# Optimization experiments

Measured on AMD Instinct MI355X. Metric: run time of the kernel, lower is better.

Reference implementation:

```python
import jax, jax.numpy as jnp
import numpy as np

GATE_SLOPE = 10.0
ALPHA = 0.8


def setup_inputs() -> dict:
    key = jax.random.key(0)
    k0, k1, k2, k3, k4, k5 = jax.random.split(key, 6)
    B, I, O, NB = 512, 128, 64, 8
    x = jax.random.normal(k0, (B, I), dtype=jnp.float32)
    k = jax.random.uniform(k1, (I, O, NB), dtype=jnp.float32) * 2.0 + 0.5
    Ec = jax.random.uniform(k2, (I, O, NB), dtype=jnp.float32) * 2.0 + 0.5
    Ps = jax.random.uniform(k3, (I, O, NB), dtype=jnp.float32) * 1.5 + 0.5
    bias = jax.random.normal(k4, (I, O, NB), dtype=jnp.float32) * 0.1
    coef = jax.random.normal(k5, (I, O, NB), dtype=jnp.float32)
    return {"x": x, "k": k, "Ec": Ec, "Ps": Ps, "bias": bias, "coef": coef}


def reference(x, k, Ec, Ps, bias, coef):
    # x: [B, I]; params: [I, O, NB]
    xe = x[:, :, None, None]  # [B, I, 1, 1], broadcasts against [I, O, NB]
    # The torch loop writes prev_x = x_sample each iteration, so sample b sees
    # x[b-1] as prev (x[-1] = 0 from the initial buffer). branch_sign is never
    # written back, so branch_snap == 1 always. prev is detached in torch.
    prev = jnp.concatenate([jnp.zeros_like(xe[:1]), xe[:-1]], axis=0)
    prev = jax.lax.stop_gradient(prev)

    is_moving_up = jax.nn.sigmoid(GATE_SLOPE * (xe - prev))          # [B,I,1,1]
    crossed_pos = jax.nn.sigmoid(GATE_SLOPE * (xe - Ec))             # [B,I,O,NB]
    crossed_neg = jax.nn.sigmoid(GATE_SLOPE * (-xe - Ec))            # [B,I,O,NB]
    switch_up = is_moving_up * crossed_pos
    switch_lo = (1.0 - is_moving_up) * crossed_neg
    # target = su*1 + sl*(-1) + (1 - su - sl)*branch_snap, branch_snap = 1
    target = switch_up - switch_lo + (1.0 - switch_up - switch_lo)
    branch_momentum = ALPHA + (1.0 - ALPHA) * target                 # alpha*1 + (1-alpha)*target
    basis = Ps * jnp.tanh(k * (xe + Ec * branch_momentum)) + bias    # [B,I,O,NB]
    return jnp.einsum('bion,ion->bo', basis, coef)                   # sum over (I, NB)
```

## Files before the change

### kernel.cpp

```cpp
#include <hip/hip_runtime.h>


#define GATE_C 14.426950408889634f
#define TANH_C 2.8853900817779268f

typedef float f32x2 __attribute__((ext_vector_type(2)));
typedef float f32x4 __attribute__((ext_vector_type(4)));
typedef int   i32x2 __attribute__((ext_vector_type(2)));

constexpr int B = 512, I = 128, O = 64, NB = 8, BT = 32, TILES = 2;
constexpr int BP = BT / 2;

__device__ __forceinline__ f32x2 pk_rcp1(f32x2 d) {
  i32x2 yi = (i32x2)(0x7EF127EA) - __builtin_bit_cast(i32x2, d);
  f32x2 y = __builtin_bit_cast(f32x2, yi);
  return y * __builtin_elementwise_fma(-d, y, (f32x2)(2.f));
}
__device__ __forceinline__ f32x2 pk_rcp2(f32x2 d) {
  i32x2 yi = (i32x2)(0x7EF127EA) - __builtin_bit_cast(i32x2, d);
  f32x2 y = __builtin_bit_cast(f32x2, yi);
  y = y * __builtin_elementwise_fma(-d, y, (f32x2)(2.f));
  return y * __builtin_elementwise_fma(-d, y, (f32x2)(2.f));
}
__device__ __forceinline__ f32x2 pk_exp2s(f32x2 t) {
  f32x2 r;
  r.x = __int_as_float((int)fmaf(t.x, 8388608.f, 1064866805.f));
  r.y = __int_as_float((int)fmaf(t.y, 8388608.f, 1064866805.f));
  return r;
}

__global__ __launch_bounds__(1024, 4) void fe_main(
    const float* __restrict__ x, const float* __restrict__ k,
    const float* __restrict__ Ec, const float* __restrict__ Ps,
    const float* __restrict__ bias, const float* __restrict__ coef,
    float* __restrict__ out)
{
  __shared__ f32x4 pl[I][NB];
  __shared__ f32x4 xp[I][BP];
  __shared__ f32x4 racc[16][8];
  __shared__ float red[16];

  const int tid = threadIdx.x;
  const int o   = blockIdx.y;
  const int n   = tid & 7;
  const int bpl = (tid >> 3) & 7;
  const int w   = tid >> 6;

  {
    const int i = tid >> 3, nn = tid & 7;
    const int g = (i * O + o) * NB + nn;
    const float E = Ec[g], K = k[g], P = Ps[g], C = coef[g], Bs = bias[g];
    const float pc = P * C;
    pl[i][nn] = (f32x4){E, E * GATE_C, K * TANH_C, pc};
    float pbase = fmaf(Bs, C, pc);
    #pragma unroll
    for (int m = 1; m < 64; m <<= 1) pbase += __shfl_xor(pbase, m);
    if ((tid & 63) == 0) red[w] = pbase;
  }

  #define PAIR(ACC, Q) {                                                     \
    const f32x2 xx = Q.lo, cc = Q.hi;                                        \
    const f32x2 ta = __builtin_elementwise_fma(xx, (f32x2)(GATE_C),          \
                                               (f32x2)(p.y));                \
    const f32x2 d1 = pk_exp2s(ta) + (f32x2)(1.f);                            \
    const f32x2 sg = pk_rcp1(d1);                    \
    const f32x2 bm = __builtin_elementwise_fma(cc, sg, (f32x2)(1.f));        \
    const f32x2 inr = __builtin_elementwise_fma((f32x2)(p.x), bm, xx);       \
    const f32x2 tb = (f32x2)(p.z) * inr;                                     \
    const f32x2 d2 = pk_exp2s(tb) + (f32x2)(1.f);                            \
    const f32x2 r = pk_rcp2(d2);                                             \
    ACC = __builtin_elementwise_fma((f32x2)(p.w), r, ACC); }

  for (int t = 0; t < TILES; ++t) {
    const int b0 = blockIdx.x * (BT * TILES) + t * BT;
    __syncthreads();

    for (int e = tid; e < I * BP; e += 1024) {
      const int bq = e & 15, i = e >> 4;
      const int re = b0 + 2 * bq;
      const float xe = x[re * I + i];
      const float xo = x[(re + 1) * I + i];
      const float xm = (re == 0) ? 0.f : x[(re - 1) * I + i];
      const float ce = -0.4f * __builtin_amdgcn_rcpf(
          1.f + __builtin_amdgcn_exp2f(GATE_C * (xe - xm)));
      const float co = -0.4f * __builtin_amdgcn_rcpf(
          1.f + __builtin_amdgcn_exp2f(GATE_C * (xo - xe)));
      xp[i][bq] = (f32x4){xe, xo, ce, co};
    }
    __syncthreads();

    f32x2 accL = (f32x2)(0.f), accH = (f32x2)(0.f);
    #pragma unroll
    for (int it = 0; it < 8; ++it) {
      const int i = w * 8 + it;
      const f32x4 p  = pl[i][n];
      const f32x4 qL = xp[i][bpl];
      const f32x4 qH = xp[i][bpl + 8];
      PAIR(accL, qL)
      PAIR(accH, qH)
    }

    #pragma unroll
    for (int m = 1; m < 8; m <<= 1) {
      accL.x += __shfl_xor(accL.x, m); accL.y += __shfl_xor(accL.y, m);
      accH.x += __shfl_xor(accH.x, m); accH.y += __shfl_xor(accH.y, m);
    }
    if (n == 0) racc[w][bpl] = (f32x4){accL.x, accL.y, accH.x, accH.y};
    __syncthreads();

    if (tid < 32) {
      const int pr = tid >> 1, sel = tid & 1;
      const int bq = pr & 7, hi = (pr >> 3) * 2;
      float s = 0.f;
      #pragma unroll
      for (int ww = 0; ww < 16; ++ww)
        s += ((const float*)&racc[ww][bq])[hi + sel];
      float base = 0.f;
      #pragma unroll
      for (int q = 0; q < 16; ++q) base += red[q];
      out[(b0 + tid) * O + o] = fmaf(-2.f, s, base);
    }
  }
  #undef PAIR
}

extern "C" void kernel_launch(void* const* d_in, const int* in_sizes, int n_in,
                              void* d_out, int out_size, void* d_ws, size_t ws_size,
                              hipStream_t stream) {
  const float* x    = (const float*)d_in[0];
  const float* k    = (const float*)d_in[1];
  const float* Ec   = (const float*)d_in[2];
  const float* Ps   = (const float*)d_in[3];
  const float* bias = (const float*)d_in[4];
  const float* coef = (const float*)d_in[5];
  float* out = (float*)d_out;

  dim3 grid(B / (BT * TILES), O);
  fe_main<<<grid, 1024, 0, stream>>>(x, k, Ec, Ps, bias, coef, out);
}
```

Baseline: 26.00 us.

## Double-buffer x tiles with register prefetch and process four tiles per block

Each block now handles four batch tiles instead of two, so the per-block parameter staging and base reduction are spread over more work. The x tile and its gate terms go into a double-buffered shared array: loads for the next tile are issued into registers before the current compute, then written to the other buffer afterwards. This removes one barrier per tile and hides global-load latency behind compute. In exchange the grid is halved, which leaves fewer blocks per CU, and the kernel uses more shared memory and registers.

```diff
diff --git a/kernel.cpp b/kernel.cpp
--- a/kernel.cpp
+++ b/kernel.cpp
@@ -8,7 +8,7 @@
 typedef float f32x4 __attribute__((ext_vector_type(4)));
 typedef int   i32x2 __attribute__((ext_vector_type(2)));
 
-constexpr int B = 512, I = 128, O = 64, NB = 8, BT = 32, TILES = 2;
+constexpr int B = 512, I = 128, O = 64, NB = 8, BT = 32, TILES = 4;
 constexpr int BP = BT / 2;
 
 __device__ __forceinline__ f32x2 pk_rcp1(f32x2 d) {
@@ -36,12 +36,13 @@
     float* __restrict__ out)
 {
   __shared__ f32x4 pl[I][NB];
-  __shared__ f32x4 xp[I][BP];
-  __shared__ f32x4 racc[16][8];
+  __shared__ f32x4 xp[2][I][BP];
+  __shared__ f32x4 racc[2][16][8];
   __shared__ float red[16];
 
   const int tid = threadIdx.x;
   const int o   = blockIdx.y;
+  const int bbase = blockIdx.x * (BT * TILES);
   const int n   = tid & 7;
   const int bpl = (tid >> 3) & 7;
   const int w   = tid >> 6;
@@ -58,6 +59,27 @@
     if ((tid & 63) == 0) red[w] = pbase;
   }
 
+  const int sbq = tid & 15;
+  const int si0 = tid >> 4;
+  const int si1 = si0 + 64;
+
+  {
+    #pragma unroll
+    for (int h = 0; h < 2; ++h) {
+      const int i = h ? si1 : si0;
+      const int re = bbase + 2 * sbq;
+      const float xe = x[re * I + i];
+      const float xo = x[(re + 1) * I + i];
+      const float xm = (re == 0) ? 0.f : x[(re - 1) * I + i];
+      const float ce = -0.4f * __builtin_amdgcn_rcpf(
+          1.f + __builtin_amdgcn_exp2f(GATE_C * (xe - xm)));
+      const float co = -0.4f * __builtin_amdgcn_rcpf(
+          1.f + __builtin_amdgcn_exp2f(GATE_C * (xo - xe)));
+      xp[0][i][sbq] = (f32x4){xe, xo, ce, co};
+    }
+  }
+  __syncthreads();
+
   #define PAIR(ACC, Q) {                                                     \
     const f32x2 xx = Q.lo, cc = Q.hi;                                        \
     const f32x2 ta = __builtin_elementwise_fma(xx, (f32x2)(GATE_C),          \
@@ -72,30 +94,24 @@
     ACC = __builtin_elementwise_fma((f32x2)(p.w), r, ACC); }
 
   for (int t = 0; t < TILES; ++t) {
-    const int b0 = blockIdx.x * (BT * TILES) + t * BT;
-    __syncthreads();
+    const int cur = t & 1;
 
-    for (int e = tid; e < I * BP; e += 1024) {
-      const int bq = e & 15, i = e >> 4;
-      const int re = b0 + 2 * bq;
-      const float xe = x[re * I + i];
-      const float xo = x[(re + 1) * I + i];
-      const float xm = (re == 0) ? 0.f : x[(re - 1) * I + i];
-      const float ce = -0.4f * __builtin_amdgcn_rcpf(
-          1.f + __builtin_amdgcn_exp2f(GATE_C * (xe - xm)));
-      const float co = -0.4f * __builtin_amdgcn_rcpf(
-          1.f + __builtin_amdgcn_exp2f(GATE_C * (xo - xe)));
-      xp[i][bq] = (f32x4){xe, xo, ce, co};
+    float pxe0, pxo0, pxm0, pxe1, pxo1, pxm1;
+    if (t + 1 < TILES) {
+      const int re = bbase + (t + 1) * BT + 2 * sbq;
+      pxe0 = x[re * I + si0]; pxo0 = x[(re + 1) * I + si0];
+      pxm0 = x[(re - 1) * I + si0];
+      pxe1 = x[re * I + si1]; pxo1 = x[(re + 1) * I + si1];
+      pxm1 = x[(re - 1) * I + si1];
     }
-    __syncthreads();
 
     f32x2 accL = (f32x2)(0.f), accH = (f32x2)(0.f);
     #pragma unroll
     for (int it = 0; it < 8; ++it) {
       const int i = w * 8 + it;
       const f32x4 p  = pl[i][n];
-      const f32x4 qL = xp[i][bpl];
-      const f32x4 qH = xp[i][bpl + 8];
+      const f32x4 qL = xp[cur][i][bpl];
+      const f32x4 qH = xp[cur][i][bpl + 8];
       PAIR(accL, qL)
       PAIR(accH, qH)
     }
@@ -105,7 +121,21 @@
       accL.x += __shfl_xor(accL.x, m); accL.y += __shfl_xor(accL.y, m);
       accH.x += __shfl_xor(accH.x, m); accH.y += __shfl_xor(accH.y, m);
     }
-    if (n == 0) racc[w][bpl] = (f32x4){accL.x, accL.y, accH.x, accH.y};
+    if (n == 0) racc[cur][w][bpl] = (f32x4){accL.x, accL.y, accH.x, accH.y};
+
+    if (t + 1 < TILES) {
+      const float ce0 = -0.4f * __builtin_amdgcn_rcpf(
+          1.f + __builtin_amdgcn_exp2f(GATE_C * (pxe0 - pxm0)));
+      const float co0 = -0.4f * __builtin_amdgcn_rcpf(
+          1.f + __builtin_amdgcn_exp2f(GATE_C * (pxo0 - pxe0)));
+      xp[cur ^ 1][si0][sbq] = (f32x4){pxe0, pxo0, ce0, co0};
+      const float ce1 = -0.4f * __builtin_amdgcn_rcpf(
+          1.f + __builtin_amdgcn_exp2f(GATE_C * (pxe1 - pxm1)));
+      const float co1 = -0.4f * __builtin_amdgcn_rcpf(
+          1.f + __builtin_amdgcn_exp2f(GATE_C * (pxo1 - pxe1)));
+      xp[cur ^ 1][si1][sbq] = (f32x4){pxe1, pxo1, ce1, co1};
+    }
+
     __syncthreads();
 
     if (tid < 32) {
@@ -114,11 +144,11 @@
       float s = 0.f;
       #pragma unroll
       for (int ww = 0; ww < 16; ++ww)
-        s += ((const float*)&racc[ww][bq])[hi + sel];
+        s += ((const float*)&racc[cur][ww][bq])[hi + sel];
       float base = 0.f;
       #pragma unroll
       for (int q = 0; q < 16; ++q) base += red[q];
-      out[(b0 + tid) * O + o] = fmaf(-2.f, s, base);
+      out[(bbase + t * BT + tid) * O + o] = fmaf(-2.f, s, base);
     }
   }
   #undef PAIR
```

Result: faster. 24.58 us (-5.4%).

## Remap threads to keep per-input params in registers and batch 8 rows per thread

Applied to the files above, without the earlier changes.

Threads are remapped so each one owns an input index i and holds all 8 basis parameter sets in registers. It then loops over 8 batch rows read from a compact shared-memory x/gate array, rather than reloading the param quad from LDS for every pair. The two-tile loop is merged into one 64-row tile per block, and the reduction becomes a full wave shuffle followed by a small cross-wave add. Occupancy drops (launch bounds go from 4 to 2), register pressure rises, and the gate sigmoid now uses the approximate exp/rcp with a clamp.

```diff
diff --git a/kernel.cpp b/kernel.cpp
--- a/kernel.cpp
+++ b/kernel.cpp
@@ -8,8 +8,7 @@
 typedef float f32x4 __attribute__((ext_vector_type(4)));
 typedef int   i32x2 __attribute__((ext_vector_type(2)));
 
-constexpr int B = 512, I = 128, O = 64, NB = 8, BT = 32, TILES = 2;
-constexpr int BP = BT / 2;
+constexpr int B = 512, I = 128, O = 64, NB = 8, BT = 64;
 
 __device__ __forceinline__ f32x2 pk_rcp1(f32x2 d) {
   i32x2 yi = (i32x2)(0x7EF127EA) - __builtin_bit_cast(i32x2, d);
@@ -28,100 +27,109 @@
   r.y = __int_as_float((int)fmaf(t.y, 8388608.f, 1064866805.f));
   return r;
 }
+__device__ __forceinline__ float s_exp2s(float t) {
+  return __int_as_float((int)fmaf(t, 8388608.f, 1064866805.f));
+}
+__device__ __forceinline__ float s_rcp1(float d) {
+  float y = __int_as_float(0x7EF127EA - __float_as_int(d));
+  return y * fmaf(-d, y, 2.f);
+}
 
-__global__ __launch_bounds__(1024, 4) void fe_main(
+__global__ __launch_bounds__(1024, 2) void fe_main(
     const float* __restrict__ x, const float* __restrict__ k,
     const float* __restrict__ Ec, const float* __restrict__ Ps,
     const float* __restrict__ bias, const float* __restrict__ coef,
     float* __restrict__ out)
 {
-  __shared__ f32x4 pl[I][NB];
-  __shared__ f32x4 xp[I][BP];
-  __shared__ f32x4 racc[16][8];
+  __shared__ f32x4 pl[NB][I];
+  __shared__ float2 xc[BT][I];
+  __shared__ float racc[16][8];
   __shared__ float red[16];
 
   const int tid = threadIdx.x;
-  const int o   = blockIdx.y;
-  const int n   = tid & 7;
-  const int bpl = (tid >> 3) & 7;
-  const int w   = tid >> 6;
+  const int o  = blockIdx.y;
+  const int b0 = blockIdx.x * BT;
+  const int w  = tid >> 6;
 
   {
-    const int i = tid >> 3, nn = tid & 7;
-    const int g = (i * O + o) * NB + nn;
+    const int i = tid >> 3, n = tid & 7;
+    const int g = (i * O + o) * NB + n;
     const float E = Ec[g], K = k[g], P = Ps[g], C = coef[g], Bs = bias[g];
     const float pc = P * C;
-    pl[i][nn] = (f32x4){E, E * GATE_C, K * TANH_C, pc};
+    pl[n][i] = (f32x4){E, E * GATE_C, K * TANH_C, pc};
     float pbase = fmaf(Bs, C, pc);
     #pragma unroll
     for (int m = 1; m < 64; m <<= 1) pbase += __shfl_xor(pbase, m);
     if ((tid & 63) == 0) red[w] = pbase;
   }
 
-  #define PAIR(ACC, Q) {                                                     \
-    const f32x2 xx = Q.lo, cc = Q.hi;                                        \
-    const f32x2 ta = __builtin_elementwise_fma(xx, (f32x2)(GATE_C),          \
-                                               (f32x2)(p.y));                \
-    const f32x2 d1 = pk_exp2s(ta) + (f32x2)(1.f);                            \
-    const f32x2 sg = pk_rcp1(d1);                    \
-    const f32x2 bm = __builtin_elementwise_fma(cc, sg, (f32x2)(1.f));        \
-    const f32x2 inr = __builtin_elementwise_fma((f32x2)(p.x), bm, xx);       \
-    const f32x2 tb = (f32x2)(p.z) * inr;                                     \
-    const f32x2 d2 = pk_exp2s(tb) + (f32x2)(1.f);                            \
-    const f32x2 r = pk_rcp2(d2);                                             \
-    ACC = __builtin_elementwise_fma((f32x2)(p.w), r, ACC); }
+  for (int e = tid; e < BT * I; e += 1024) {
+    const int bb = e >> 7, i = e & 127;
+    const int bg = b0 + bb;
+    const float xv = x[bg * I + i];
+    const float pv = (bg == 0) ? 0.f : x[(bg - 1) * I + i];
+    const float tg = fminf(GATE_C * (xv - pv), 120.f);
+    const float ch = -0.4f * s_rcp1(1.f + s_exp2s(tg));
+    xc[bb][i] = make_float2(xv, ch);
+  }
+  __syncthreads();
 
-  for (int t = 0; t < TILES; ++t) {
-    const int b0 = blockIdx.x * (BT * TILES) + t * BT;
-    __syncthreads();
+  const int i0 = tid & 127, bslot = tid >> 7;
+  const f32x4 q0 = pl[0][i0], q1 = pl[1][i0], q2 = pl[2][i0], q3 = pl[3][i0];
+  const f32x4 q4 = pl[4][i0], q5 = pl[5][i0], q6 = pl[6][i0], q7 = pl[7][i0];
+  const f32x2 ec0 = {q0.x, q1.x}, gg0 = {q0.y, q1.y},
+              kt0 = {q0.z, q1.z}, pc0 = {q0.w, q1.w};
+  const f32x2 ec1 = {q2.x, q3.x}, gg1 = {q2.y, q3.y},
+              kt1 = {q2.z, q3.z}, pc1 = {q2.w, q3.w};
+  const f32x2 ec2 = {q4.x, q5.x}, gg2 = {q4.y, q5.y},
+              kt2 = {q4.z, q5.z}, pc2 = {q4.w, q5.w};
+  const f32x2 ec3 = {q6.x, q7.x}, gg3 = {q6.y, q7.y},
+              kt3 = {q6.z, q7.z}, pc3 = {q6.w, q7.w};
 
-    for (int e = tid; e < I * BP; e += 1024) {
-      const int bq = e & 15, i = e >> 4;
-      const int re = b0 + 2 * bq;
-      const float xe = x[re * I + i];
-      const float xo = x[(re + 1) * I + i];
-      const float xm = (re == 0) ? 0.f : x[(re - 1) * I + i];
-      const float ce = -0.4f * __builtin_amdgcn_rcpf(
-          1.f + __builtin_amdgcn_exp2f(GATE_C * (xe - xm)));
-      const float co = -0.4f * __builtin_amdgcn_rcpf(
-          1.f + __builtin_amdgcn_exp2f(GATE_C * (xo - xe)));
-      xp[i][bq] = (f32x4){xe, xo, ce, co};
-    }
-    __syncthreads();
+  #define NPAIR(ACC, ECQ, GGQ, KTQ, PCQ) {                                  \
+    const f32x2 ta = __builtin_elementwise_fma(xx, (f32x2)(GATE_C), GGQ);   \
+    const f32x2 d1 = pk_exp2s(ta) + (f32x2)(1.f);                           \
+    const f32x2 sg = pk_rcp1(d1);                   \
+    const f32x2 bm = __builtin_elementwise_fma(cc, sg, (f32x2)(1.f));       \
+    const f32x2 inr = __builtin_elementwise_fma(ECQ, bm, xx);               \
+    const f32x2 tb = KTQ * inr;                                             \
+    const f32x2 d2 = pk_exp2s(tb) + (f32x2)(1.f);                           \
+    ACC = __builtin_elementwise_fma(PCQ, pk_rcp2(d2), ACC); }
 
-    f32x2 accL = (f32x2)(0.f), accH = (f32x2)(0.f);
+  #define ROWB(AJ, J) {                                                     \
+    const float2 v = xc[bslot * 8 + (J)][i0];                               \
+    const f32x2 xx = (f32x2)(v.x);                                          \
+    const f32x2 cc = (f32x2)(v.y);                                          \
+    NPAIR(AJ, ec0, gg0, kt0, pc0)                                           \
+    NPAIR(AJ, ec1, gg1, kt1, pc1)                                           \
+    NPAIR(AJ, ec2, gg2, kt2, pc2)                                           \
+    NPAIR(AJ, ec3, gg3, kt3, pc3) }
+
+  f32x2 a0 = (f32x2)(0.f), a1 = (f32x2)(0.f), a2 = (f32x2)(0.f),
+        a3 = (f32x2)(0.f), a4 = (f32x2)(0.f), a5 = (f32x2)(0.f),
+        a6 = (f32x2)(0.f), a7 = (f32x2)(0.f);
+  ROWB(a0, 0) ROWB(a1, 1) ROWB(a2, 2) ROWB(a3, 3)
+  ROWB(a4, 4) ROWB(a5, 5) ROWB(a6, 6) ROWB(a7, 7)
+
+  #define RED(AJ, J) { float s = AJ.x + AJ.y;                               \
+    s += __shfl_xor(s, 1);  s += __shfl_xor(s, 2);  s += __shfl_xor(s, 4);  \
+    s += __shfl_xor(s, 8);  s += __shfl_xor(s, 16); s += __shfl_xor(s, 32); \
+    if ((tid & 63) == 0) racc[w][J] = s; }
+  RED(a0, 0) RED(a1, 1) RED(a2, 2) RED(a3, 3)
+  RED(a4, 4) RED(a5, 5) RED(a6, 6) RED(a7, 7)
+  __syncthreads();
+
+  if (tid < BT) {
+    const int bs = tid >> 3, j = tid & 7;
+    const float s = racc[bs * 2][j] + racc[bs * 2 + 1][j];
+    float base = 0.f;
     #pragma unroll
-    for (int it = 0; it < 8; ++it) {
-      const int i = w * 8 + it;
-      const f32x4 p  = pl[i][n];
-      const f32x4 qL = xp[i][bpl];
-      const f32x4 qH = xp[i][bpl + 8];
-      PAIR(accL, qL)
-      PAIR(accH, qH)
-    }
-
-    #pragma unroll
-    for (int m = 1; m < 8; m <<= 1) {
-      accL.x += __shfl_xor(accL.x, m); accL.y += __shfl_xor(accL.y, m);
-      accH.x += __shfl_xor(accH.x, m); accH.y += __shfl_xor(accH.y, m);
-    }
-    if (n == 0) racc[w][bpl] = (f32x4){accL.x, accL.y, accH.x, accH.y};
-    __syncthreads();
-
-    if (tid < 32) {
-      const int pr = tid >> 1, sel = tid & 1;
-      const int bq = pr & 7, hi = (pr >> 3) * 2;
-      float s = 0.f;
-      #pragma unroll
-      for (int ww = 0; ww < 16; ++ww)
-        s += ((const float*)&racc[ww][bq])[hi + sel];
-      float base = 0.f;
-      #pragma unroll
-      for (int q = 0; q < 16; ++q) base += red[q];
-      out[(b0 + tid) * O + o] = fmaf(-2.f, s, base);
-    }
+    for (int q = 0; q < 16; ++q) base += red[q];
+    out[(b0 + tid) * O + o] = fmaf(-2.f, s, base);
   }
-  #undef PAIR
+  #undef NPAIR
+  #undef ROWB
+  #undef RED
 }
 
 extern "C" void kernel_launch(void* const* d_in, const int* in_sizes, int n_in,
@@ -135,6 +143,6 @@
   const float* coef = (const float*)d_in[5];
   float* out = (float*)d_out;
 
-  dim3 grid(B / (BT * TILES), O);
+  dim3 grid(B / BT, O);
   fe_main<<<grid, 1024, 0, stream>>>(x, k, Ec, Ps, bias, coef, out);
 }
```

After: 26.12 us. Within noise of the previous version (+0.5%).
